# Performance work log

Hardware: AMD Instinct MI355X
Metric: run time of the kernel (lower is better)

The kernel has to match this reference:

```python
import jax, jax.numpy as jnp
import numpy as np

T = 2048      # tokens
H = 1024      # hidden_size
HQ = 16       # num query heads
HK = 4        # num kv heads
D = 64        # head_dim
E = 8         # num experts
K = 2         # top_k
I = 2048      # expert intermediate size
EPS = 1e-5
THETA = 10000.0


def setup_inputs() -> dict:
    key = jax.random.key(0)
    ks = jax.random.split(key, 8)
    s = 0.02
    return {
        "hidden_states": jax.random.normal(ks[0], (T, H), jnp.float32),
        "positions": jnp.arange(T, dtype=jnp.int32),
        "qkv_w": jax.random.normal(ks[1], ((HQ + 2 * HK) * D, H), jnp.float32) * s,
        "o_w": jax.random.normal(ks[2], (H, HQ * D), jnp.float32) * s,
        "norm_in_w": jnp.ones((H,), jnp.float32),
        "norm_post_w": jnp.ones((H,), jnp.float32),
        "norm_next_w": jnp.ones((H,), jnp.float32),
        "gate_w": jax.random.normal(ks[3], (E, H), jnp.float32) * s,
        "w1": jax.random.normal(ks[4], (E, I, H), jnp.float32) * s,
        "w3": jax.random.normal(ks[5], (E, I, H), jnp.float32) * s,
        "w2": jax.random.normal(ks[6], (E, H, I), jnp.float32) * s,
    }


def rmsnorm(x, w):
    var = jnp.mean(x * x, axis=-1, keepdims=True)
    return x * jax.lax.rsqrt(var + EPS) * w


def rope_neox(x, positions):
    # x: [T, nH, D]; rotate-half (neox) style
    half = D // 2
    inv_freq = 1.0 / (THETA ** (jnp.arange(0, half, dtype=jnp.float32) * 2.0 / D))
    ang = positions.astype(jnp.float32)[:, None] * inv_freq[None, :]      # [T, D/2]
    cos = jnp.cos(ang)[:, None, :]
    sin = jnp.sin(ang)[:, None, :]
    x1, x2 = x[..., :half], x[..., half:]
    return jnp.concatenate([x1 * cos - x2 * sin, x2 * cos + x1 * sin], axis=-1)


def reference(hidden_states, positions, qkv_w, o_w, norm_in_w, norm_post_w,
              norm_next_w, gate_w, w1, w3, w2):
    x = hidden_states                               # [T, H]
    residual = x
    h = rmsnorm(x, norm_in_w)                       # input_layernorm

    # ---- attention (GQA, causal, neox RoPE) ----
    qkv = h @ qkv_w.T                               # [T, (HQ+2HK)*D]
    q, k, v = jnp.split(qkv, [HQ * D, (HQ + HK) * D], axis=-1)
    q = rope_neox(q.reshape(T, HQ, D), positions)
    k = rope_neox(k.reshape(T, HK, D), positions)
    v = v.reshape(T, HK, D)
    rep = HQ // HK
    k = jnp.repeat(k, rep, axis=1)                  # [T, HQ, D]
    v = jnp.repeat(v, rep, axis=1)
    scale = D ** -0.5
    scores = jnp.einsum('qhd,khd->hqk', q, k) * scale   # [HQ, T, T]
    mask = jnp.tril(jnp.ones((T, T), dtype=bool))
    scores = jnp.where(mask[None], scores, -jnp.inf)
    probs = jax.nn.softmax(scores, axis=-1)
    attn = jnp.einsum('hqk,khd->qhd', probs, v).reshape(T, HQ * D)
    attn_out = attn @ o_w.T                         # [T, H]

    # fused allreduce(identity, world=1) + residual add + post_attention RMSNorm
    residual = residual + attn_out
    h = rmsnorm(residual, norm_post_w)

    # ---- MoE: gate, top-2, renormalize, SiLU-gated experts ----
    logits = h @ gate_w.T                           # [T, E]
    route = jax.nn.softmax(logits, axis=-1)
    topw, topi = jax.lax.top_k(route, K)            # [T, K]
    topw = topw / jnp.sum(topw, axis=-1, keepdims=True)   # renormalize
    # dense combine weights [T, E] (zero for unselected experts)
    wdense = jnp.sum(jax.nn.one_hot(topi, E, dtype=h.dtype) * topw[..., None], axis=1)
    h1 = jnp.einsum('td,eid->tei', h, w1)           # [T, E, I]
    h3 = jnp.einsum('td,eid->tei', h, w3)
    gated = jax.nn.silu(h1) * h3
    moe_out = jnp.einsum('tei,edi,te->td', gated, w2, wdense)   # [T, H]

    # fused allreduce(identity) + residual add + next layer norm
    residual = residual + moe_out
    h = rmsnorm(residual, norm_next_w)
    return h
```

## Files before the change

kernel.cpp:

```cpp
#include <hip/hip_runtime.h>
#include <hip/hip_bf16.h>
#include <math.h>

#define T_ 2048
#define H_ 1024
#define HQ_ 16
#define HK_ 4
#define D_ 64
#define NE_ 8
#define II_ 2048

typedef __attribute__((ext_vector_type(8))) short bf16x8;
typedef __attribute__((ext_vector_type(8))) unsigned short u16x8;
typedef __attribute__((ext_vector_type(4))) float f32x4;

#define GLOAD16(g, l)                                                                   \
  __builtin_amdgcn_global_load_lds((const __attribute__((address_space(1))) unsigned int*)(g), \
                                   (__attribute__((address_space(3))) unsigned int*)(l), 16, 0, 0)

__device__ __forceinline__ unsigned short f2bf(float f) {
  unsigned int u = __float_as_uint(f);
  return (unsigned short)((u + 0x7fffu + ((u >> 16) & 1u)) >> 16);
}
__device__ __forceinline__ float bf2f(unsigned short h) {
  return __uint_as_float((unsigned int)h << 16);
}

__global__ __launch_bounds__(256) void k_rmsnorm(const float* __restrict__ x, const float* __restrict__ w,
                                                 float* __restrict__ outf, unsigned short* __restrict__ outb) {
  int row = blockIdx.x;
  int tid = threadIdx.x;
  float4 v = ((const float4*)(x + (size_t)row * H_))[tid];
  float ss = v.x * v.x + v.y * v.y + v.z * v.z + v.w * v.w;
#pragma unroll
  for (int off = 32; off; off >>= 1) ss += __shfl_xor(ss, off, 64);
  __shared__ float red[4];
  int lane = tid & 63, wid = tid >> 6;
  if (lane == 0) red[wid] = ss;
  __syncthreads();
  float tot = red[0] + red[1] + red[2] + red[3];
  float inv = rsqrtf(tot * (1.0f / H_) + 1e-5f);
  float4 wv = ((const float4*)w)[tid];
  float4 o;
  o.x = v.x * inv * wv.x; o.y = v.y * inv * wv.y; o.z = v.z * inv * wv.z; o.w = v.w * inv * wv.w;
  ((float4*)(outf + (size_t)row * H_))[tid] = o;
  if (outb) {
    ushort4 b; b.x = f2bf(o.x); b.y = f2bf(o.y); b.z = f2bf(o.z); b.w = f2bf(o.w);
    ((ushort4*)(outb + (size_t)row * H_))[tid] = b;
  }
}

__global__ __launch_bounds__(256) void k_rmsnorm_split(const float* __restrict__ x, const float* __restrict__ w,
                                                       unsigned short* __restrict__ Aq) {
  int row = blockIdx.x;
  int tid = threadIdx.x;
  float4 v = ((const float4*)(x + (size_t)row * H_))[tid];
  float ss = v.x * v.x + v.y * v.y + v.z * v.z + v.w * v.w;
#pragma unroll
  for (int off = 32; off; off >>= 1) ss += __shfl_xor(ss, off, 64);
  __shared__ float red[4];
  int lane = tid & 63, wid = tid >> 6;
  if (lane == 0) red[wid] = ss;
  __syncthreads();
  float tot = red[0] + red[1] + red[2] + red[3];
  float inv = rsqrtf(tot * (1.0f / H_) + 1e-5f);
  float4 wv = ((const float4*)w)[tid];
  float4 o;
  o.x = v.x * inv * wv.x; o.y = v.y * inv * wv.y; o.z = v.z * inv * wv.z; o.w = v.w * inv * wv.w;
  ushort4 hi, lo;
  hi.x = f2bf(o.x); hi.y = f2bf(o.y); hi.z = f2bf(o.z); hi.w = f2bf(o.w);
  lo.x = f2bf(o.x - bf2f(hi.x)); lo.y = f2bf(o.y - bf2f(hi.y));
  lo.z = f2bf(o.z - bf2f(hi.z)); lo.w = f2bf(o.w - bf2f(hi.w));
  size_t base = (size_t)row * (3 * H_) + tid * 4;
  *(ushort4*)(Aq + base) = hi;
  *(ushort4*)(Aq + base + H_) = hi;
  *(ushort4*)(Aq + base + 2 * H_) = lo;
}

__global__ __launch_bounds__(256) void k_wsplit(const float* __restrict__ in, unsigned short* __restrict__ out,
                                                int K, int n8total) {
  int stride = gridDim.x * 256;
  int kc8 = K >> 3;
  for (int i = blockIdx.x * 256 + threadIdx.x; i < n8total; i += stride) {
    int n = i / kc8, kc = (i - n * kc8) * 8;
    const float4* p = (const float4*)(in + (size_t)n * K + kc);
    float4 a = p[0], b = p[1];
    u16x8 hi, lo;
    hi[0] = f2bf(a.x); hi[1] = f2bf(a.y); hi[2] = f2bf(a.z); hi[3] = f2bf(a.w);
    hi[4] = f2bf(b.x); hi[5] = f2bf(b.y); hi[6] = f2bf(b.z); hi[7] = f2bf(b.w);
    lo[0] = f2bf(a.x - bf2f(hi[0])); lo[1] = f2bf(a.y - bf2f(hi[1]));
    lo[2] = f2bf(a.z - bf2f(hi[2])); lo[3] = f2bf(a.w - bf2f(hi[3]));
    lo[4] = f2bf(b.x - bf2f(hi[4])); lo[5] = f2bf(b.y - bf2f(hi[5]));
    lo[6] = f2bf(b.z - bf2f(hi[6])); lo[7] = f2bf(b.w - bf2f(hi[7]));
    size_t ob = (size_t)n * 3 * K + kc;
    *(u16x8*)(out + ob) = hi;
    *(u16x8*)(out + ob + K) = lo;
    *(u16x8*)(out + ob + 2 * K) = hi;
  }
}

template <int ADD>
__global__ __launch_bounds__(256) void k_hgemm(const unsigned short* __restrict__ A, const unsigned short* __restrict__ B,
                                               float* __restrict__ C, const float* __restrict__ addsrc,
                                               int N, int K3) {
  int m0 = blockIdx.y * 128, n0 = blockIdx.x * 64;
  __shared__ unsigned short As[2][128 * 32];
  __shared__ unsigned short Bs[2][64 * 32];
  int tid = threadIdx.x, lane = tid & 63, w = tid >> 6;
  int wr = w >> 1, wc = w & 1;
  int l15 = lane & 15, lg = lane >> 4;
  int srow = lane >> 2, schunk = lane & 3;

  const unsigned short* ga0 = A + (size_t)(m0 + w * 32 + srow) * K3 + schunk * 8;
  const unsigned short* ga1 = A + (size_t)(m0 + w * 32 + 16 + srow) * K3 + schunk * 8;
  const unsigned short* gb = B + (size_t)(n0 + w * 16 + srow) * K3 + schunk * 8;

  f32x4 acc[4][2];
  f32x4 z = {0.f, 0.f, 0.f, 0.f};
#pragma unroll
  for (int a = 0; a < 4; a++)
#pragma unroll
    for (int b = 0; b < 2; b++) acc[a][b] = z;

  GLOAD16(ga0, &As[0][(w * 32) * 32]);
  GLOAD16(ga1, &As[0][(w * 32 + 16) * 32]);
  GLOAD16(gb, &Bs[0][(w * 16) * 32]);
  __syncthreads();

  int nt = K3 / 32;
  for (int t = 0; t < nt; ++t) {
    int cur = t & 1;
    if (t + 1 < nt) {
      int ko = (t + 1) * 32;
      GLOAD16(ga0 + ko, &As[cur ^ 1][(w * 32) * 32]);
      GLOAD16(ga1 + ko, &As[cur ^ 1][(w * 32 + 16) * 32]);
      GLOAD16(gb + ko, &Bs[cur ^ 1][(w * 16) * 32]);
    }
    bf16x8 af[4], bw2[2];
#pragma unroll
    for (int fa = 0; fa < 4; fa++)
      af[fa] = *(const bf16x8*)&As[cur][(wr * 64 + fa * 16 + l15) * 32 + lg * 8];
#pragma unroll
    for (int fb = 0; fb < 2; fb++)
      bw2[fb] = *(const bf16x8*)&Bs[cur][(wc * 32 + fb * 16 + l15) * 32 + lg * 8];
#pragma unroll
    for (int fa = 0; fa < 4; fa++)
#pragma unroll
      for (int fb = 0; fb < 2; fb++)
        acc[fa][fb] = __builtin_amdgcn_mfma_f32_16x16x32_bf16(af[fa], bw2[fb], acc[fa][fb], 0, 0, 0);
    __syncthreads();
  }
#pragma unroll
  for (int fa = 0; fa < 4; fa++)
#pragma unroll
    for (int r = 0; r < 4; r++) {
      int row = m0 + wr * 64 + fa * 16 + lg * 4 + r;
#pragma unroll
      for (int fb = 0; fb < 2; fb++) {
        int col = n0 + wc * 32 + fb * 16 + l15;
        float v = acc[fa][fb][r];
        if (ADD) v += addsrc[(size_t)row * N + col];
        C[(size_t)row * N + col] = v;
      }
    }
}

__global__ __launch_bounds__(256) void k_rope_table(const int* __restrict__ pos, float* __restrict__ ct,
                                                    float* __restrict__ st) {
  int idx = blockIdx.x * 256 + threadIdx.x;
  int t = idx >> 5, i = idx & 31;
  float p = (float)pow(10000.0, (double)i / 32.0);
  float freq = 1.0f / p;
  float ang = (float)pos[t] * freq;
  ct[idx] = cosf(ang);
  st[idx] = sinf(ang);
}

__global__ __launch_bounds__(256) void k_rope_prep(const float* __restrict__ qkv, const float* __restrict__ ct,
                                                   const float* __restrict__ st, unsigned short* __restrict__ Qhi,
                                                   unsigned short* __restrict__ Qlo, unsigned short* __restrict__ Khi,
                                                   unsigned short* __restrict__ Klo) {
  int t = blockIdx.x, tid = threadIdx.x;
  const float* row = qkv + (size_t)t * 1536;
#pragma unroll 2
  for (int it = tid; it < 512; it += 256) {
    int h = it >> 5, i = it & 31;
    float c = ct[t * 32 + i], s = st[t * 32 + i];
    float x1 = row[h * 64 + i], x2 = row[h * 64 + i + 32];
    float a = (x1 * c - x2 * s) * 0.125f;
    float b = (x2 * c + x1 * s) * 0.125f;
    size_t base = ((size_t)h * T_ + t) * 64 + i;
    unsigned short ah = f2bf(a), bh = f2bf(b);
    Qhi[base] = ah; Qhi[base + 32] = bh;
    Qlo[base] = f2bf(a - bf2f(ah));
    Qlo[base + 32] = f2bf(b - bf2f(bh));
  }
  if (tid < 128) {
    int h = tid >> 5, i = tid & 31;
    float c = ct[t * 32 + i], s = st[t * 32 + i];
    float x1 = row[1024 + h * 64 + i], x2 = row[1024 + h * 64 + i + 32];
    float a = x1 * c - x2 * s;
    float b = x2 * c + x1 * s;
    size_t base = ((size_t)h * T_ + t) * 64 + i;
    unsigned short ah = f2bf(a), bh = f2bf(b);
    Khi[base] = ah; Khi[base + 32] = bh;
    Klo[base] = f2bf(a - bf2f(ah));
    Klo[base + 32] = f2bf(b - bf2f(bh));
  }
}

__global__ __launch_bounds__(256) void k_vtrans(const float* __restrict__ qkv, unsigned short* __restrict__ Vthi,
                                                unsigned short* __restrict__ Vtlo) {
  int t0 = blockIdx.x * 64, h = blockIdx.y;
  __shared__ float tile[64][65];
  int tid = threadIdx.x;
  int c = tid & 63, w = tid >> 6;
  for (int r = w; r < 64; r += 4)
    tile[r][c] = qkv[(size_t)(t0 + r) * 1536 + 1280 + h * 64 + c];
  __syncthreads();
  for (int d = w; d < 64; d += 4) {
    float v = tile[c][d];
    unsigned short hi = f2bf(v);
    size_t idx = ((size_t)h * 64 + d) * T_ + t0 + c;
    Vthi[idx] = hi;
    Vtlo[idx] = f2bf(v - bf2f(hi));
  }
}

__global__ __launch_bounds__(256) void k_attn_mfma(const unsigned short* __restrict__ Qhi,
                                                   const unsigned short* __restrict__ Qlo,
                                                   const unsigned short* __restrict__ Khi,
                                                   const unsigned short* __restrict__ Klo,
                                                   const unsigned short* __restrict__ Vthi,
                                                   const unsigned short* __restrict__ Vtlo,
                                                   unsigned short* __restrict__ Ao) {
  int bid = blockIdx.x;
  int kk = bid >> 4;
  int head = bid & 15;
  int qidx = (kk < 16) ? (31 - kk) : (kk - 16);
  int qb = qidx * 64;
  int kvh = head >> 2;
  int tid = threadIdx.x, lane = tid & 63, w = tid >> 6;
  int l15 = lane & 15, lg = lane >> 4;

  __shared__ unsigned short S[4 * 64 * 72];
  unsigned short* KsH = S;
  unsigned short* KsL = S + 4608;
  unsigned short* VsH = S + 9216;
  unsigned short* VsL = S + 13824;
  unsigned short* PsH = KsH;
  unsigned short* PsL = KsL;

  bf16x8 qh[2], ql[2];
  {
    size_t qbase = ((size_t)head * T_ + qb + w * 16 + l15) * 64 + lg * 8;
    qh[0] = *(const bf16x8*)(Qhi + qbase);
    qh[1] = *(const bf16x8*)(Qhi + qbase + 32);
    ql[0] = *(const bf16x8*)(Qlo + qbase);
    ql[1] = *(const bf16x8*)(Qlo + qbase + 32);
  }
  f32x4 z = {0.f, 0.f, 0.f, 0.f};
  f32x4 Oa[4];
  float mrow[4], lrow[4];
#pragma unroll
  for (int r = 0; r < 4; r++) { mrow[r] = -1e30f; lrow[r] = 0.f; }
#pragma unroll
  for (int dg = 0; dg < 4; dg++) Oa[dg] = z;

  for (int jb = 0; jb <= qb; jb += 64) {
    for (int c = tid; c < 512; c += 256) {
      int r = c >> 3, g = (c & 7) * 8;
      size_t kgl = ((size_t)kvh * T_ + jb + r) * 64 + g;
      size_t vgl = ((size_t)kvh * 64 + r) * T_ + jb + g;
      *(uint4*)&KsH[r * 72 + g] = *(const uint4*)(Khi + kgl);
      *(uint4*)&KsL[r * 72 + g] = *(const uint4*)(Klo + kgl);
      *(uint4*)&VsH[r * 72 + g] = *(const uint4*)(Vthi + vgl);
      *(uint4*)&VsL[r * 72 + g] = *(const uint4*)(Vtlo + vgl);
    }
    __syncthreads();

    f32x4 sc[4];
    sc[0] = z; sc[1] = z; sc[2] = z; sc[3] = z;
#pragma unroll
    for (int kg = 0; kg < 4; kg++) {
      int ba = (kg * 16 + l15) * 72 + lg * 8;
      bf16x8 bh0 = *(const bf16x8*)&KsH[ba];
      bf16x8 bh1 = *(const bf16x8*)&KsH[ba + 32];
      bf16x8 bl0 = *(const bf16x8*)&KsL[ba];
      bf16x8 bl1 = *(const bf16x8*)&KsL[ba + 32];
      sc[kg] = __builtin_amdgcn_mfma_f32_16x16x32_bf16(qh[0], bh0, sc[kg], 0, 0, 0);
      sc[kg] = __builtin_amdgcn_mfma_f32_16x16x32_bf16(qh[1], bh1, sc[kg], 0, 0, 0);
      sc[kg] = __builtin_amdgcn_mfma_f32_16x16x32_bf16(qh[0], bl0, sc[kg], 0, 0, 0);
      sc[kg] = __builtin_amdgcn_mfma_f32_16x16x32_bf16(qh[1], bl1, sc[kg], 0, 0, 0);
      sc[kg] = __builtin_amdgcn_mfma_f32_16x16x32_bf16(ql[0], bh0, sc[kg], 0, 0, 0);
      sc[kg] = __builtin_amdgcn_mfma_f32_16x16x32_bf16(ql[1], bh1, sc[kg], 0, 0, 0);
    }
    if (jb == qb) {
      int rb = w * 16 + lg * 4;
#pragma unroll
      for (int kg = 0; kg < 4; kg++) {
        int col = kg * 16 + l15;
#pragma unroll
        for (int r = 0; r < 4; r++)
          if (col > rb + r) sc[kg][r] = -1e30f;
      }
    }
#pragma unroll
    for (int r = 0; r < 4; r++) {
      float mt = fmaxf(fmaxf(sc[0][r], sc[1][r]), fmaxf(sc[2][r], sc[3][r]));
      mt = fmaxf(mt, __shfl_xor(mt, 1, 64));
      mt = fmaxf(mt, __shfl_xor(mt, 2, 64));
      mt = fmaxf(mt, __shfl_xor(mt, 4, 64));
      mt = fmaxf(mt, __shfl_xor(mt, 8, 64));
      float mnew = fmaxf(mrow[r], mt);
      float corr = __expf(mrow[r] - mnew);
      mrow[r] = mnew;
      float s = 0.f;
#pragma unroll
      for (int kg = 0; kg < 4; kg++) {
        float p = __expf(sc[kg][r] - mnew);
        sc[kg][r] = p;
        s += p;
      }
      s += __shfl_xor(s, 1, 64);
      s += __shfl_xor(s, 2, 64);
      s += __shfl_xor(s, 4, 64);
      s += __shfl_xor(s, 8, 64);
      lrow[r] = lrow[r] * corr + s;
#pragma unroll
      for (int dg = 0; dg < 4; dg++) Oa[dg][r] *= corr;
    }
    __syncthreads();
    {
      int rb = w * 16 + lg * 4;
#pragma unroll
      for (int kg = 0; kg < 4; kg++) {
        int col = kg * 16 + l15;
#pragma unroll
        for (int r = 0; r < 4; r++) {
          float p = sc[kg][r];
          unsigned short ph = f2bf(p);
          PsH[(rb + r) * 72 + col] = ph;
          PsL[(rb + r) * 72 + col] = f2bf(p - bf2f(ph));
        }
      }
    }
    {
      int ab = (w * 16 + l15) * 72 + lg * 8;
      bf16x8 ph0 = *(const bf16x8*)&PsH[ab];
      bf16x8 ph1 = *(const bf16x8*)&PsH[ab + 32];
      bf16x8 pl0 = *(const bf16x8*)&PsL[ab];
      bf16x8 pl1 = *(const bf16x8*)&PsL[ab + 32];
#pragma unroll
      for (int dg = 0; dg < 4; dg++) {
        int vb = (dg * 16 + l15) * 72 + lg * 8;
        bf16x8 vh0 = *(const bf16x8*)&VsH[vb];
        bf16x8 vh1 = *(const bf16x8*)&VsH[vb + 32];
        bf16x8 vl0 = *(const bf16x8*)&VsL[vb];
        bf16x8 vl1 = *(const bf16x8*)&VsL[vb + 32];
        Oa[dg] = __builtin_amdgcn_mfma_f32_16x16x32_bf16(ph0, vh0, Oa[dg], 0, 0, 0);
        Oa[dg] = __builtin_amdgcn_mfma_f32_16x16x32_bf16(ph1, vh1, Oa[dg], 0, 0, 0);
        Oa[dg] = __builtin_amdgcn_mfma_f32_16x16x32_bf16(ph0, vl0, Oa[dg], 0, 0, 0);
        Oa[dg] = __builtin_amdgcn_mfma_f32_16x16x32_bf16(ph1, vl1, Oa[dg], 0, 0, 0);
        Oa[dg] = __builtin_amdgcn_mfma_f32_16x16x32_bf16(pl0, vh0, Oa[dg], 0, 0, 0);
        Oa[dg] = __builtin_amdgcn_mfma_f32_16x16x32_bf16(pl1, vh1, Oa[dg], 0, 0, 0);
      }
    }
    __syncthreads();
  }
#pragma unroll
  for (int r = 0; r < 4; r++) {
    float inv = 1.0f / lrow[r];
    size_t rb2 = (size_t)(qb + w * 16 + lg * 4 + r) * 3072 + head * 64;
#pragma unroll
    for (int dg = 0; dg < 4; dg++) {
      float v = Oa[dg][r] * inv;
      unsigned short hi2 = f2bf(v);
      unsigned short lo2 = f2bf(v - bf2f(hi2));
      Ao[rb2 + dg * 16 + l15] = hi2;
      Ao[rb2 + 1024 + dg * 16 + l15] = hi2;
      Ao[rb2 + 2048 + dg * 16 + l15] = lo2;
    }
  }
}

__global__ __launch_bounds__(256) void k_router(const float* __restrict__ h2, const float* __restrict__ gw,
                                                int* __restrict__ topi, float* __restrict__ topw,
                                                int* __restrict__ counts) {
  int wid = threadIdx.x >> 6, lane = threadIdx.x & 63;
  int t = blockIdx.x * 4 + wid;
  const float* hr = h2 + (size_t)t * H_;
  float hv[16];
#pragma unroll
  for (int i = 0; i < 16; i++) hv[i] = hr[lane + 64 * i];
  float le[8];
#pragma unroll
  for (int e = 0; e < 8; e++) {
    const float* g = gw + (size_t)e * H_;
    float acc = 0.f;
#pragma unroll
    for (int i = 0; i < 16; i++) acc += hv[i] * g[lane + 64 * i];
#pragma unroll
    for (int off = 32; off; off >>= 1) acc += __shfl_xor(acc, off, 64);
    le[e] = acc;
  }
  if (lane == 0) {
    int i0 = 0;
#pragma unroll
    for (int e = 1; e < 8; e++)
      if (le[e] > le[i0]) i0 = e;
    int i1 = (i0 == 0) ? 1 : 0;
#pragma unroll
    for (int e = 0; e < 8; e++) {
      if (e == i0) continue;
      if (le[e] > le[i1]) i1 = e;
    }
    float w1r = expf(le[i1] - le[i0]);
    float denom = 1.0f + w1r;
    topi[t * 2 + 0] = i0;
    topi[t * 2 + 1] = i1;
    topw[t * 2 + 0] = 1.0f / denom;
    topw[t * 2 + 1] = w1r / denom;
    atomicAdd(&counts[i0], 1);
    atomicAdd(&counts[i1], 1);
  }
}

__global__ void k_scan(const int* __restrict__ counts, int* __restrict__ offsets) {
  if (threadIdx.x == 0 && blockIdx.x == 0) {
    int off = 0;
    for (int e = 0; e < NE_; e++) { offsets[e] = off; off += counts[e]; }
  }
}

__global__ __launch_bounds__(256) void k_build(const int* __restrict__ topi, const float* __restrict__ topw,
                                               const int* __restrict__ offsets, int* __restrict__ counts2,
                                               int* __restrict__ pairs_ts, float* __restrict__ pairs_w) {
  int t = blockIdx.x * 256 + threadIdx.x;
#pragma unroll
  for (int s = 0; s < 2; s++) {
    int e = topi[t * 2 + s];
    int slot = atomicAdd(&counts2[e], 1);
    int p = offsets[e] + slot;
    pairs_ts[p] = t * 2 + s;
    pairs_w[p] = topw[t * 2 + s];
  }
}

__global__ __launch_bounds__(256) void k_conv(const float* __restrict__ in, unsigned short* __restrict__ out, int n8) {
  int stride = gridDim.x * 256;
  for (int i = blockIdx.x * 256 + threadIdx.x; i < n8; i += stride) {
    const float4* p = (const float4*)in + (size_t)i * 2;
    float4 a = p[0], b = p[1];
    u16x8 t;
    t[0] = f2bf(a.x); t[1] = f2bf(a.y); t[2] = f2bf(a.z); t[3] = f2bf(a.w);
    t[4] = f2bf(b.x); t[5] = f2bf(b.y); t[6] = f2bf(b.z); t[7] = f2bf(b.w);
    *((u16x8*)out + i) = t;
  }
}

__global__ __launch_bounds__(256) void k_moe_up(const unsigned short* __restrict__ h2b, const unsigned short* __restrict__ W1b,
                                                const unsigned short* __restrict__ W3b, const int* __restrict__ pairs_ts,
                                                const int* __restrict__ offsets, const int* __restrict__ counts,
                                                unsigned short* __restrict__ G) {
  int e = blockIdx.z;
  int ne = counts[e];
  int row0 = blockIdx.y * 128;
  if (row0 >= ne) return;
  int col0 = blockIdx.x * 64;
  int pbase = offsets[e];
  __shared__ unsigned short As[2][128 * 32];
  __shared__ unsigned short B1s[2][64 * 32];
  __shared__ unsigned short B2s[2][64 * 32];
  int tid = threadIdx.x, lane = tid & 63, w = tid >> 6;
  int wr = w >> 1, wc = w & 1;
  int l15 = lane & 15, lg = lane >> 4;
  int srow = lane >> 2, schunk = lane & 3;

  int gr0 = row0 + w * 32 + srow, gr1 = gr0 + 16;
  int tok0 = (gr0 < ne) ? (pairs_ts[pbase + gr0] >> 1) : 0;
  int tok1 = (gr1 < ne) ? (pairs_ts[pbase + gr1] >> 1) : 0;
  const unsigned short* ga0 = h2b + (size_t)tok0 * H_ + schunk * 8;
  const unsigned short* ga1 = h2b + (size_t)tok1 * H_ + schunk * 8;
  const unsigned short* gb1 = W1b + ((size_t)e * II_ + col0 + w * 16 + srow) * H_ + schunk * 8;
  const unsigned short* gb3 = W3b + ((size_t)e * II_ + col0 + w * 16 + srow) * H_ + schunk * 8;

  f32x4 acc1[4][2], acc2[4][2];
  f32x4 z = {0.f, 0.f, 0.f, 0.f};
#pragma unroll
  for (int a = 0; a < 4; a++)
#pragma unroll
    for (int b = 0; b < 2; b++) { acc1[a][b] = z; acc2[a][b] = z; }

  GLOAD16(ga0, &As[0][(w * 32) * 32]);
  GLOAD16(ga1, &As[0][(w * 32 + 16) * 32]);
  GLOAD16(gb1, &B1s[0][(w * 16) * 32]);
  GLOAD16(gb3, &B2s[0][(w * 16) * 32]);
  __syncthreads();

  for (int t = 0; t < H_ / 32; ++t) {
    int cur = t & 1;
    if (t + 1 < H_ / 32) {
      int ko = (t + 1) * 32;
      GLOAD16(ga0 + ko, &As[cur ^ 1][(w * 32) * 32]);
      GLOAD16(ga1 + ko, &As[cur ^ 1][(w * 32 + 16) * 32]);
      GLOAD16(gb1 + ko, &B1s[cur ^ 1][(w * 16) * 32]);
      GLOAD16(gb3 + ko, &B2s[cur ^ 1][(w * 16) * 32]);
    }
    bf16x8 af[4], b1f[2], b2f[2];
#pragma unroll
    for (int fa = 0; fa < 4; fa++)
      af[fa] = *(const bf16x8*)&As[cur][(wr * 64 + fa * 16 + l15) * 32 + lg * 8];
#pragma unroll
    for (int fb = 0; fb < 2; fb++) {
      b1f[fb] = *(const bf16x8*)&B1s[cur][(wc * 32 + fb * 16 + l15) * 32 + lg * 8];
      b2f[fb] = *(const bf16x8*)&B2s[cur][(wc * 32 + fb * 16 + l15) * 32 + lg * 8];
    }
#pragma unroll
    for (int fa = 0; fa < 4; fa++)
#pragma unroll
      for (int fb = 0; fb < 2; fb++) {
        acc1[fa][fb] = __builtin_amdgcn_mfma_f32_16x16x32_bf16(af[fa], b1f[fb], acc1[fa][fb], 0, 0, 0);
        acc2[fa][fb] = __builtin_amdgcn_mfma_f32_16x16x32_bf16(af[fa], b2f[fb], acc2[fa][fb], 0, 0, 0);
      }
    __syncthreads();
  }
#pragma unroll
  for (int fa = 0; fa < 4; fa++)
#pragma unroll
    for (int r = 0; r < 4; r++) {
      int prow = row0 + wr * 64 + fa * 16 + lg * 4 + r;
      if (prow < ne) {
#pragma unroll
        for (int fb = 0; fb < 2; fb++) {
          int icol = col0 + wc * 32 + fb * 16 + l15;
          float h1 = acc1[fa][fb][r], h3 = acc2[fa][fb][r];
          float g = h1 / (1.0f + __expf(-h1)) * h3;
          G[(size_t)(pbase + prow) * II_ + icol] = f2bf(g);
        }
      }
    }
}

__global__ __launch_bounds__(256) void k_moe_down(const unsigned short* __restrict__ G, const unsigned short* __restrict__ W2b,
                                                  const int* __restrict__ pairs_ts, const float* __restrict__ pairs_w,
                                                  const int* __restrict__ offsets, const int* __restrict__ counts,
                                                  float* __restrict__ Pbuf) {
  int e = blockIdx.z;
  int ne = counts[e];
  int row0 = blockIdx.y * 128;
  if (row0 >= ne) return;
  int col0 = blockIdx.x * 64;
  int pbase = offsets[e];
  __shared__ unsigned short As[2][128 * 32];
  __shared__ unsigned short Bs[2][64 * 32];
  int tid = threadIdx.x, lane = tid & 63, w = tid >> 6;
  int wr = w >> 1, wc = w & 1;
  int l15 = lane & 15, lg = lane >> 4;
  int srow = lane >> 2, schunk = lane & 3;

  int gr0 = row0 + w * 32 + srow, gr1 = gr0 + 16;
  int p0 = pbase + ((gr0 < ne) ? gr0 : 0);
  int p1 = pbase + ((gr1 < ne) ? gr1 : 0);
  const unsigned short* ga0 = G + (size_t)p0 * II_ + schunk * 8;
  const unsigned short* ga1 = G + (size_t)p1 * II_ + schunk * 8;
  const unsigned short* gb = W2b + ((size_t)e * H_ + col0 + w * 16 + srow) * II_ + schunk * 8;

  f32x4 acc[4][2];
  f32x4 z = {0.f, 0.f, 0.f, 0.f};
#pragma unroll
  for (int a = 0; a < 4; a++)
#pragma unroll
    for (int b = 0; b < 2; b++) acc[a][b] = z;

  GLOAD16(ga0, &As[0][(w * 32) * 32]);
  GLOAD16(ga1, &As[0][(w * 32 + 16) * 32]);
  GLOAD16(gb, &Bs[0][(w * 16) * 32]);
  __syncthreads();

  for (int t = 0; t < II_ / 32; ++t) {
    int cur = t & 1;
    if (t + 1 < II_ / 32) {
      int ko = (t + 1) * 32;
      GLOAD16(ga0 + ko, &As[cur ^ 1][(w * 32) * 32]);
      GLOAD16(ga1 + ko, &As[cur ^ 1][(w * 32 + 16) * 32]);
      GLOAD16(gb + ko, &Bs[cur ^ 1][(w * 16) * 32]);
    }
    bf16x8 af[4], bw2[2];
#pragma unroll
    for (int fa = 0; fa < 4; fa++)
      af[fa] = *(const bf16x8*)&As[cur][(wr * 64 + fa * 16 + l15) * 32 + lg * 8];
#pragma unroll
    for (int fb = 0; fb < 2; fb++)
      bw2[fb] = *(const bf16x8*)&Bs[cur][(wc * 32 + fb * 16 + l15) * 32 + lg * 8];
#pragma unroll
    for (int fa = 0; fa < 4; fa++)
#pragma unroll
      for (int fb = 0; fb < 2; fb++)
        acc[fa][fb] = __builtin_amdgcn_mfma_f32_16x16x32_bf16(af[fa], bw2[fb], acc[fa][fb], 0, 0, 0);
    __syncthreads();
  }
#pragma unroll
  for (int fa = 0; fa < 4; fa++)
#pragma unroll
    for (int r = 0; r < 4; r++) {
      int prow = row0 + wr * 64 + fa * 16 + lg * 4 + r;
      if (prow < ne) {
        int p = pbase + prow;
        int ts = pairs_ts[p];
        float wgt = pairs_w[p];
#pragma unroll
        for (int fb = 0; fb < 2; fb++) {
          int col = col0 + wc * 32 + fb * 16 + l15;
          Pbuf[(size_t)ts * H_ + col] = wgt * acc[fa][fb][r];
        }
      }
    }
}

__global__ __launch_bounds__(256) void k_final(const float* __restrict__ resid, const float* __restrict__ Pbuf,
                                               const float* __restrict__ w, float* __restrict__ out) {
  int row = blockIdx.x;
  int tid = threadIdx.x;
  float4 a = ((const float4*)(resid + (size_t)row * H_))[tid];
  float4 p0 = ((const float4*)(Pbuf + (size_t)(2 * row) * H_))[tid];
  float4 p1 = ((const float4*)(Pbuf + (size_t)(2 * row + 1) * H_))[tid];
  float4 v;
  v.x = a.x + p0.x + p1.x; v.y = a.y + p0.y + p1.y; v.z = a.z + p0.z + p1.z; v.w = a.w + p0.w + p1.w;
  float ss = v.x * v.x + v.y * v.y + v.z * v.z + v.w * v.w;
#pragma unroll
  for (int off = 32; off; off >>= 1) ss += __shfl_xor(ss, off, 64);
  __shared__ float red[4];
  int lane = tid & 63, wid = tid >> 6;
  if (lane == 0) red[wid] = ss;
  __syncthreads();
  float tot = red[0] + red[1] + red[2] + red[3];
  float inv = rsqrtf(tot * (1.0f / H_) + 1e-5f);
  float4 wv = ((const float4*)w)[tid];
  float4 o;
  o.x = v.x * inv * wv.x; o.y = v.y * inv * wv.y; o.z = v.z * inv * wv.z; o.w = v.w * inv * wv.w;
  ((float4*)(out + (size_t)row * H_))[tid] = o;
}

extern "C" void kernel_launch(void* const* d_in, const int* in_sizes, int n_in,
                              void* d_out, int out_size, void* d_ws, size_t ws_size,
                              hipStream_t stream) {
  const float* x = (const float*)d_in[0];
  const int* pos = (const int*)d_in[1];
  const float* qkv_w = (const float*)d_in[2];
  const float* o_w = (const float*)d_in[3];
  const float* nin_w = (const float*)d_in[4];
  const float* npost_w = (const float*)d_in[5];
  const float* nnext_w = (const float*)d_in[6];
  const float* gate_w = (const float*)d_in[7];
  const float* w1 = (const float*)d_in[8];
  const float* w3 = (const float*)d_in[9];
  const float* w2 = (const float*)d_in[10];
  float* out = (float*)d_out;

  float* resid = (float*)d_ws;
  float* h2 = resid + (size_t)T_ * H_;
  float* Pbuf = h2 + (size_t)T_ * H_;
  float* topw = Pbuf + (size_t)2 * T_ * H_;
  float* pairsw = topw + T_ * 2;
  unsigned short* h2b = (unsigned short*)(pairsw + 4096);
  unsigned short* G = h2b + (size_t)T_ * H_;
  int* topi = (int*)(G + (size_t)2 * T_ * II_);
  int* ctrl = topi + T_ * 2;
  int* counts = ctrl;
  int* counts2 = ctrl + 8;
  int* offsets = ctrl + 16;
  int* pairs_ts = ctrl + 24;
  char* trans = (char*)(pairs_ts + 4096);
  trans = (char*)(((uintptr_t)trans + 255) & ~(uintptr_t)255);

  unsigned short* Aq = (unsigned short*)trans;
  unsigned short* Bq = Aq + (size_t)T_ * 3072;
  unsigned short* Bo = Bq + (size_t)1536 * 3072;
  unsigned short* Ao = Bo + (size_t)1024 * 3072;
  float* qkvb = (float*)(Ao + (size_t)T_ * 3072);
  float* ct = qkvb + (size_t)T_ * 1536;
  float* st = ct + (size_t)T_ * 32;
  unsigned short* uu = (unsigned short*)(st + (size_t)T_ * 32);
  unsigned short* Qhi = uu;  uu += (size_t)HQ_ * T_ * D_;
  unsigned short* Qlo = uu;  uu += (size_t)HQ_ * T_ * D_;
  unsigned short* Khi = uu;  uu += (size_t)HK_ * T_ * D_;
  unsigned short* Klo = uu;  uu += (size_t)HK_ * T_ * D_;
  unsigned short* Vthi = uu; uu += (size_t)HK_ * D_ * T_;
  unsigned short* Vtlo = uu; uu += (size_t)HK_ * D_ * T_;

  unsigned short* W1b = (unsigned short*)trans;
  unsigned short* W3b = W1b + (size_t)NE_ * II_ * H_;
  unsigned short* W2b = W3b + (size_t)NE_ * II_ * H_;

  const int WCNT8 = (NE_ * II_ * H_) / 8;

  hipMemsetAsync(ctrl, 0, 64, stream);
  k_rmsnorm_split<<<T_, 256, 0, stream>>>(x, nin_w, Aq);
  k_wsplit<<<2048, 256, 0, stream>>>(qkv_w, Bq, H_, 1536 * H_ / 8);
  k_wsplit<<<2048, 256, 0, stream>>>(o_w, Bo, HQ_ * D_, H_ * HQ_ * D_ / 8);
  k_hgemm<0><<<dim3(1536 / 64, T_ / 128), 256, 0, stream>>>(Aq, Bq, qkvb, nullptr, 1536, 3 * H_);
  k_rope_table<<<T_ * 32 / 256, 256, 0, stream>>>(pos, ct, st);
  k_rope_prep<<<T_, 256, 0, stream>>>(qkvb, ct, st, Qhi, Qlo, Khi, Klo);
  k_vtrans<<<dim3(T_ / 64, HK_), 256, 0, stream>>>(qkvb, Vthi, Vtlo);
  k_attn_mfma<<<dim3(512), 256, 0, stream>>>(Qhi, Qlo, Khi, Klo, Vthi, Vtlo, Ao);
  k_hgemm<1><<<dim3(H_ / 64, T_ / 128), 256, 0, stream>>>(Ao, Bo, resid, x, H_, 3 * HQ_ * D_);
  k_rmsnorm<<<T_, 256, 0, stream>>>(resid, npost_w, h2, h2b);
  k_router<<<T_ / 4, 256, 0, stream>>>(h2, gate_w, topi, topw, counts);
  k_scan<<<1, 64, 0, stream>>>(counts, offsets);
  k_build<<<T_ / 256, 256, 0, stream>>>(topi, topw, offsets, counts2, pairs_ts, pairsw);
  k_conv<<<2048, 256, 0, stream>>>(w1, W1b, WCNT8);
  k_conv<<<2048, 256, 0, stream>>>(w3, W3b, WCNT8);
  k_conv<<<2048, 256, 0, stream>>>(w2, W2b, WCNT8);
  k_moe_up<<<dim3(II_ / 64, T_ / 128, NE_), 256, 0, stream>>>(h2b, W1b, W3b, pairs_ts, offsets, counts, G);
  k_moe_down<<<dim3(H_ / 64, T_ / 128, NE_), 256, 0, stream>>>(G, W2b, pairs_ts, pairsw, offsets, counts, Pbuf);
  k_final<<<T_, 256, 0, stream>>>(resid, Pbuf, nnext_w, out);
}
```

Baseline: 489.8 us.

## Make attention waves independent, loading K/V straight from global memory

The attention kernel no longer stages K/V tiles in shared memory with block-wide barriers. Each wave now owns 16 query rows and reads its K and transposed-V fragments directly from global memory (relying on cache reuse across waves). It loops only over the key tiles its own rows need under the causal mask, and keeps a private LDS slice for the P matrix. This removes all __syncthreads and the causal over-compute of the 64-row block granularity. In exchange, each wave issues redundant global loads with exposed latency and no prefetch.

```diff
diff --git a/kernel.cpp b/kernel.cpp
--- a/kernel.cpp
+++ b/kernel.cpp
@@ -237,23 +237,21 @@
   int bid = blockIdx.x;
   int kk = bid >> 4;
   int head = bid & 15;
-  int qidx = (kk < 16) ? (31 - kk) : (kk - 16);
-  int qb = qidx * 64;
+  int q4 = 31 - kk;
+  int tid = threadIdx.x, lane = tid & 63, w = tid >> 6;
+  int q128 = q4 * 4 + w;
+  int qb16 = q128 * 16;
   int kvh = head >> 2;
-  int tid = threadIdx.x, lane = tid & 63, w = tid >> 6;
   int l15 = lane & 15, lg = lane >> 4;
 
-  __shared__ unsigned short S[4 * 64 * 72];
-  unsigned short* KsH = S;
-  unsigned short* KsL = S + 4608;
-  unsigned short* VsH = S + 9216;
-  unsigned short* VsL = S + 13824;
-  unsigned short* PsH = KsH;
-  unsigned short* PsL = KsL;
+  __shared__ unsigned short PsH[4][16 * 72];
+  __shared__ unsigned short PsL[4][16 * 72];
+  unsigned short* psH = PsH[w];
+  unsigned short* psL = PsL[w];
 
   bf16x8 qh[2], ql[2];
   {
-    size_t qbase = ((size_t)head * T_ + qb + w * 16 + l15) * 64 + lg * 8;
+    size_t qbase = ((size_t)head * T_ + qb16 + l15) * 64 + lg * 8;
     qh[0] = *(const bf16x8*)(Qhi + qbase);
     qh[1] = *(const bf16x8*)(Qhi + qbase + 32);
     ql[0] = *(const bf16x8*)(Qlo + qbase);
@@ -267,27 +265,24 @@
 #pragma unroll
   for (int dg = 0; dg < 4; dg++) Oa[dg] = z;
 
-  for (int jb = 0; jb <= qb; jb += 64) {
-    for (int c = tid; c < 512; c += 256) {
-      int r = c >> 3, g = (c & 7) * 8;
-      size_t kgl = ((size_t)kvh * T_ + jb + r) * 64 + g;
-      size_t vgl = ((size_t)kvh * 64 + r) * T_ + jb + g;
-      *(uint4*)&KsH[r * 72 + g] = *(const uint4*)(Khi + kgl);
-      *(uint4*)&KsL[r * 72 + g] = *(const uint4*)(Klo + kgl);
-      *(uint4*)&VsH[r * 72 + g] = *(const uint4*)(Vthi + vgl);
-      *(uint4*)&VsL[r * 72 + g] = *(const uint4*)(Vtlo + vgl);
-    }
-    __syncthreads();
+  const unsigned short* kbH = Khi + ((size_t)kvh * T_ + l15) * 64 + lg * 8;
+  const unsigned short* kbL = Klo + ((size_t)kvh * T_ + l15) * 64 + lg * 8;
+  const unsigned short* vbH = Vthi + ((size_t)(kvh * 64 + l15)) * T_ + lg * 8;
+  const unsigned short* vbL = Vtlo + ((size_t)(kvh * 64 + l15)) * T_ + lg * 8;
+
+  int ntiles = (qb16 + 16 + 63) >> 6;
+  for (int jbt = 0; jbt < ntiles; ++jbt) {
+    int jb = jbt * 64;
 
     f32x4 sc[4];
     sc[0] = z; sc[1] = z; sc[2] = z; sc[3] = z;
 #pragma unroll
     for (int kg = 0; kg < 4; kg++) {
-      int ba = (kg * 16 + l15) * 72 + lg * 8;
-      bf16x8 bh0 = *(const bf16x8*)&KsH[ba];
-      bf16x8 bh1 = *(const bf16x8*)&KsH[ba + 32];
-      bf16x8 bl0 = *(const bf16x8*)&KsL[ba];
-      bf16x8 bl1 = *(const bf16x8*)&KsL[ba + 32];
+      size_t ko = (size_t)(jb + kg * 16) * 64;
+      bf16x8 bh0 = *(const bf16x8*)(kbH + ko);
+      bf16x8 bh1 = *(const bf16x8*)(kbH + ko + 32);
+      bf16x8 bl0 = *(const bf16x8*)(kbL + ko);
+      bf16x8 bl1 = *(const bf16x8*)(kbL + ko + 32);
       sc[kg] = __builtin_amdgcn_mfma_f32_16x16x32_bf16(qh[0], bh0, sc[kg], 0, 0, 0);
       sc[kg] = __builtin_amdgcn_mfma_f32_16x16x32_bf16(qh[1], bh1, sc[kg], 0, 0, 0);
       sc[kg] = __builtin_amdgcn_mfma_f32_16x16x32_bf16(qh[0], bl0, sc[kg], 0, 0, 0);
@@ -295,14 +290,13 @@
       sc[kg] = __builtin_amdgcn_mfma_f32_16x16x32_bf16(ql[0], bh0, sc[kg], 0, 0, 0);
       sc[kg] = __builtin_amdgcn_mfma_f32_16x16x32_bf16(ql[1], bh1, sc[kg], 0, 0, 0);
     }
-    if (jb == qb) {
-      int rb = w * 16 + lg * 4;
+    if (jbt == ntiles - 1) {
 #pragma unroll
       for (int kg = 0; kg < 4; kg++) {
-        int col = kg * 16 + l15;
+        int col = jb + kg * 16 + l15;
 #pragma unroll
         for (int r = 0; r < 4; r++)
-          if (col > rb + r) sc[kg][r] = -1e30f;
+          if (col > qb16 + lg * 4 + r) sc[kg][r] = -1e30f;
       }
     }
 #pragma unroll
@@ -330,9 +324,7 @@
 #pragma unroll
       for (int dg = 0; dg < 4; dg++) Oa[dg][r] *= corr;
     }
-    __syncthreads();
     {
-      int rb = w * 16 + lg * 4;
 #pragma unroll
       for (int kg = 0; kg < 4; kg++) {
         int col = kg * 16 + l15;
@@ -340,24 +332,24 @@
         for (int r = 0; r < 4; r++) {
           float p = sc[kg][r];
           unsigned short ph = f2bf(p);
-          PsH[(rb + r) * 72 + col] = ph;
-          PsL[(rb + r) * 72 + col] = f2bf(p - bf2f(ph));
+          psH[(lg * 4 + r) * 72 + col] = ph;
+          psL[(lg * 4 + r) * 72 + col] = f2bf(p - bf2f(ph));
         }
       }
     }
     {
-      int ab = (w * 16 + l15) * 72 + lg * 8;
-      bf16x8 ph0 = *(const bf16x8*)&PsH[ab];
-      bf16x8 ph1 = *(const bf16x8*)&PsH[ab + 32];
-      bf16x8 pl0 = *(const bf16x8*)&PsL[ab];
-      bf16x8 pl1 = *(const bf16x8*)&PsL[ab + 32];
+      int ab = l15 * 72 + lg * 8;
+      bf16x8 ph0 = *(const bf16x8*)&psH[ab];
+      bf16x8 ph1 = *(const bf16x8*)&psH[ab + 32];
+      bf16x8 pl0 = *(const bf16x8*)&psL[ab];
+      bf16x8 pl1 = *(const bf16x8*)&psL[ab + 32];
 #pragma unroll
       for (int dg = 0; dg < 4; dg++) {
-        int vb = (dg * 16 + l15) * 72 + lg * 8;
-        bf16x8 vh0 = *(const bf16x8*)&VsH[vb];
-        bf16x8 vh1 = *(const bf16x8*)&VsH[vb + 32];
-        bf16x8 vl0 = *(const bf16x8*)&VsL[vb];
-        bf16x8 vl1 = *(const bf16x8*)&VsL[vb + 32];
+        size_t vo = (size_t)(dg * 16) * T_ + jb;
+        bf16x8 vh0 = *(const bf16x8*)(vbH + vo);
+        bf16x8 vh1 = *(const bf16x8*)(vbH + vo + 32);
+        bf16x8 vl0 = *(const bf16x8*)(vbL + vo);
+        bf16x8 vl1 = *(const bf16x8*)(vbL + vo + 32);
         Oa[dg] = __builtin_amdgcn_mfma_f32_16x16x32_bf16(ph0, vh0, Oa[dg], 0, 0, 0);
         Oa[dg] = __builtin_amdgcn_mfma_f32_16x16x32_bf16(ph1, vh1, Oa[dg], 0, 0, 0);
         Oa[dg] = __builtin_amdgcn_mfma_f32_16x16x32_bf16(ph0, vl0, Oa[dg], 0, 0, 0);
@@ -366,12 +358,11 @@
         Oa[dg] = __builtin_amdgcn_mfma_f32_16x16x32_bf16(pl1, vh1, Oa[dg], 0, 0, 0);
       }
     }
-    __syncthreads();
   }
 #pragma unroll
   for (int r = 0; r < 4; r++) {
     float inv = 1.0f / lrow[r];
-    size_t rb2 = (size_t)(qb + w * 16 + lg * 4 + r) * 3072 + head * 64;
+    size_t rb2 = (size_t)(qb16 + lg * 4 + r) * 3072 + head * 64;
 #pragma unroll
     for (int dg = 0; dg < 4; dg++) {
       float v = Oa[dg][r] * inv;
```

New measurement: 574.0 us. 1.17x slower.
